# Kernel tuning notes

Hardware: AMD Instinct MI355X
Metric: run time of the kernel (lower is better)

The kernel has to match this reference:

```python
import jax, jax.numpy as jnp
import numpy as np

N = 100000      # nodes
E = 800000      # edges (nnz of sparse adj)
D_IN = 128      # input feature dim
H = 64          # hidden_units
EMB = 32        # embsize
N_IDX = 50000   # gathered output rows
EPS = 1e-05     # BatchNormalization epsilon


def spmm(rows, cols, vals, x):
    # out[i] = sum_{e: rows[e]==i} vals[e] * x[cols[e]]  == sparse A @ x
    return jax.ops.segment_sum(vals[:, None] * x[cols], rows, num_segments=N)


def batchnorm(x, gamma, beta):
    # training-mode BN over node (batch) axis, matching Keras BatchNormalization
    m = jnp.mean(x, axis=0)
    v = jnp.var(x, axis=0)
    return (x - m) * jax.lax.rsqrt(v + EPS) * gamma + beta


def setup_inputs() -> dict:
    key = jax.random.key(0)
    ks = jax.random.split(key, 16)
    def w(k, fan_in, shape):
        return jax.random.normal(k, shape, dtype=jnp.float32) / np.sqrt(fan_in)
    inp = {
        "features": jax.random.normal(ks[0], (N, D_IN), dtype=jnp.float32),
        "rows": jax.random.randint(ks[1], (E,), 0, N),
        "cols": jax.random.randint(ks[2], (E,), 0, N),
        "vals": jax.random.uniform(ks[3], (E,), dtype=jnp.float32),
        "idx": jax.random.randint(ks[4], (N_IDX,), 0, N),
        # layer 0 (Dense with bias since l==0)
        "Wn0": w(ks[5], D_IN, (D_IN, H)), "bn0": jnp.zeros((H,), jnp.float32),
        "Wg0": w(ks[6], D_IN, (D_IN, H)), "bg0": jnp.zeros((H,), jnp.float32),
        "ab0": jnp.zeros((H,), jnp.float32),  # BiasLayer after SpMM
        "g0": jnp.ones((H,), jnp.float32), "b0": jnp.zeros((H,), jnp.float32),
        # layer 1 (no Dense bias)
        "Wn1": w(ks[7], H, (H, H)),
        "Wg1": w(ks[8], H, (H, H)),
        "ab1": jnp.zeros((H,), jnp.float32),
        "g1": jnp.ones((H,), jnp.float32), "b1": jnp.zeros((H,), jnp.float32),
        # conv_last block (Dense use_bias=False)
        "WnL": w(ks[9], H, (H, EMB)),
        "WgL": w(ks[10], H, (H, EMB)),
        "abL": jnp.zeros((EMB,), jnp.float32),
    }
    return inp


def reference(features, rows, cols, vals, idx,
              Wn0, bn0, Wg0, bg0, ab0, g0, b0,
              Wn1, Wg1, ab1, g1, b1,
              WnL, WgL, abL):
    x = features
    # SAGE layer 0
    x_node = x @ Wn0 + bn0
    x_neigh = x @ Wg0 + bg0
    agg = spmm(rows, cols, vals, x_neigh) + ab0
    x = jax.nn.relu(batchnorm(x_node + agg, g0, b0))
    # SAGE layer 1
    x_node = x @ Wn1
    x_neigh = x @ Wg1
    agg = spmm(rows, cols, vals, x_neigh) + ab1
    x = jax.nn.relu(batchnorm(x_node + agg, g1, b1))
    # conv_last projection to embsize
    x_node = x @ WnL
    x_neigh = x @ WgL
    agg = spmm(rows, cols, vals, x_neigh) + abL
    x = x_node + agg
    return x[idx]
```

## Files before the change

### kernel.cpp

```cpp
#include <hip/hip_runtime.h>

#define NNODES 100000
#define NEDGES 800000
#define DIN    128
#define HID    64
#define EMB    32
#define NIDX   50000
#define BN_EPS 1e-5f

#define NCHK 64
#define EC   (NEDGES / NCHK)
#define SUBC 256
#define ECS  (NEDGES / SUBC)
#define SPC  (SUBC / NCHK)
#define NB   ((NNODES + 63) / 64)
#define PF   16
#define NBF  ((NB + PF - 1) / PF)

typedef __attribute__((ext_vector_type(8))) short short8;
typedef __attribute__((ext_vector_type(4))) float f32x4;

__device__ inline unsigned short f2bf(float f) {
    unsigned u = __float_as_uint(f);
    unsigned r = u + 0x7FFFu + ((u >> 16) & 1u);
    return (unsigned short)(r >> 16);
}
__device__ inline float bf2f_lo(unsigned u) { return __uint_as_float(u << 16); }
__device__ inline float bf2f_hi(unsigned u) { return __uint_as_float(u & 0xffff0000u); }


__device__ inline void pack_seg(const float* __restrict__ Wn, const float* __restrict__ Wg,
                                unsigned short* __restrict__ Wp, int HOUT, int l2nt, int f) {
    int j = f & 7, lane = (f >> 3) & 63, g = f >> 9;
    int tt = g & ((1 << l2nt) - 1), kb = g >> l2nt;
    int k = kb * 32 + ((lane >> 4) * 8) + j;
    int nn = tt * 16 + (lane & 15);
    float v = (nn < HOUT) ? Wn[k * HOUT + nn] : Wg[k * HOUT + (nn - HOUT)];
    Wp[f] = f2bf(v);
}


__global__ __launch_bounds__(256) void histpack_k(
    const int* __restrict__ rows, int* __restrict__ Bcnt4,
    const int* __restrict__ idx, int* __restrict__ mark,
    const float* Wn0, const float* Wg0, const float* Wn1,
    const float* Wg1, const float* WnL, const float* WgL,
    unsigned short* Wp0, unsigned short* Wp1, unsigned short* WpL, int MB)
{
    int blk = blockIdx.x;
    if (blk >= SUBC + MB) {
        int f = (blk - SUBC - MB) * 256 + threadIdx.x;
        if (f < 16384)      pack_seg(Wn0, Wg0, Wp0, 64, 3, f);
        else if (f < 24576) pack_seg(Wn1, Wg1, Wp1, 64, 3, f - 16384);
        else if (f < 28672) pack_seg(WnL, WgL, WpL, 32, 2, f - 24576);
        return;
    }
    if (blk >= SUBC) {
        int j = (blk - SUBC) * 256 + threadIdx.x;
        if (j < NIDX) mark[idx[j]] = 1;
        return;
    }
    __shared__ int hist[NB];
    int t = threadIdx.x;
    for (int b = t; b < NB; b += 256) hist[b] = 0;
    __syncthreads();
    for (int i = t; i < ECS; i += 256)
        atomicAdd(&hist[rows[blk * ECS + i] >> 6], 1);
    __syncthreads();
    for (int b = t; b < NB; b += 256) Bcnt4[blk * NB + b] = hist[b];
}

__global__ void bprefix_k(const int* __restrict__ Bcnt4, int* __restrict__ BcntT,
                          int* __restrict__ bTot) {
    int b = blockIdx.x * 256 + threadIdx.x;
    if (b >= NB) return;
    int run = 0;
    for (int sub = 0; sub < SUBC; sub++) {
        if ((sub & (SPC - 1)) == 0)
            BcntT[(sub / SPC) * NB + b] = run;
        run += Bcnt4[sub * NB + b];
    }
    bTot[b] = run;
}

__global__ void bscan_k(const int* __restrict__ bTot, int* __restrict__ bBase) {
    __shared__ int s[256];
    int t = threadIdx.x;
    int v[7], loc = 0;
#pragma unroll
    for (int i = 0; i < 7; i++) {
        int ix = t * 7 + i;
        v[i] = loc;
        loc += (ix < NB) ? bTot[ix] : 0;
    }
    s[t] = loc;
    __syncthreads();
    for (int off = 1; off < 256; off <<= 1) {
        int a = (t >= off) ? s[t - off] : 0;
        __syncthreads();
        s[t] += a;
        __syncthreads();
    }
    int base = s[t] - loc;
#pragma unroll
    for (int i = 0; i < 7; i++) {
        int ix = t * 7 + i;
        if (ix < NB) bBase[ix] = base + v[i];
    }
    if (t == 255) bBase[NB] = NEDGES;
}

__global__ __launch_bounds__(256) void bfinal_k(const uint2* __restrict__ ebuf,
                                                const int* __restrict__ bBase,
                                                int* __restrict__ rowptr,
                                                int2* __restrict__ cs) {
    __shared__ int hist[64], sc[64], cur[64];
    int b = blockIdx.x, t = threadIdx.x;
    int e0 = bBase[b], e1 = bBase[b + 1];
    int r0 = b << 6;
    if (t < 64) hist[t] = 0;
    __syncthreads();
    for (int i = e0 + t; i < e1; i += 256)
        atomicAdd(&hist[(ebuf[i].x >> 20) & 63], 1);
    __syncthreads();
    if (t == 0) {
        int run = e0;
        for (int j = 0; j < 64; j++) { sc[j] = run; run += hist[j]; }
    }
    __syncthreads();
    if (t < 64) {
        cur[t] = sc[t];
        int r = r0 + t;
        if (r < NNODES) rowptr[r] = sc[t];
    }
    if (b == NB - 1 && t == 0) rowptr[NNODES] = NEDGES;
    __syncthreads();
    for (int i = e0 + t; i < e1; i += 256) {
        uint2 v = ebuf[i];
        int p = atomicAdd(&cur[(v.x >> 20) & 63], 1);
        cs[p] = make_int2((int)(v.x & 0xFFFFF), (int)v.y);
    }
}


template <int K, int HOUT, bool AFF, bool XBF, bool HNBF>
__device__ void gemm_body(const void* __restrict__ Xv, const unsigned short* __restrict__ Wp,
                          const float* __restrict__ bnA, const float* __restrict__ bnB,
                          const float* __restrict__ bgA,
                          const float* __restrict__ sums, const float* __restrict__ gamma,
                          const float* __restrict__ beta,
                          float* __restrict__ Hnf, unsigned short* __restrict__ Hnb,
                          unsigned short* __restrict__ Hgb, int n, int blk)
{
    constexpr int NT = 2 * HOUT / 16, NKB = K / 32;
    constexpr int RS = K + 8;
    constexpr int OC = HNBF ? 2 * HOUT : HOUT;
    constexpr int RSE = OC + 8;
    constexpr int XSZ = (RS > RSE) ? RS : RSE;
    __shared__ unsigned short Xs[64 * XSZ];
    __shared__ float sSc[64], sSh[64];

    const int row0 = blk * 64;
    const int t = threadIdx.x;

    if (AFF) {
        if (t < 64) {
            float sum = 0.f, sq = 0.f;
#pragma unroll
            for (int s = 0; s < 8; s++) { sum += sums[s * 128 + t]; sq += sums[s * 128 + 64 + t]; }
            float m = sum / (float)NNODES;
            float var = sq / (float)NNODES - m * m;
            float sc = gamma[t] * rsqrtf(var + BN_EPS);
            sSc[t] = sc; sSh[t] = beta[t] - m * sc;
        }
        __syncthreads();
    }

    constexpr int SIT = K / 32;
    if constexpr (XBF) {
        uint4 u[SIT];
#pragma unroll
        for (int it = 0; it < SIT; it++) {
            int li = it * 256 + t;
            int rr = row0 + li / (K / 8);
            int k8 = (li % (K / 8)) * 8;
            int rc = rr < n ? rr : n - 1;
            u[it] = *(const uint4*)((const unsigned short*)Xv + (size_t)rc * K + k8);
        }
#pragma unroll
        for (int it = 0; it < SIT; it++) {
            int li = it * 256 + t;
            int r  = li / (K / 8);
            int k8 = (li % (K / 8)) * 8;
            float v[8];
            v[0] = bf2f_lo(u[it].x); v[1] = bf2f_hi(u[it].x);
            v[2] = bf2f_lo(u[it].y); v[3] = bf2f_hi(u[it].y);
            v[4] = bf2f_lo(u[it].z); v[5] = bf2f_hi(u[it].z);
            v[6] = bf2f_lo(u[it].w); v[7] = bf2f_hi(u[it].w);
            if (AFF) {
#pragma unroll
                for (int i = 0; i < 8; i++) v[i] = fmaxf(v[i] * sSc[k8 + i] + sSh[k8 + i], 0.f);
            }
            uint4 o;
            o.x = (unsigned)f2bf(v[0]) | ((unsigned)f2bf(v[1]) << 16);
            o.y = (unsigned)f2bf(v[2]) | ((unsigned)f2bf(v[3]) << 16);
            o.z = (unsigned)f2bf(v[4]) | ((unsigned)f2bf(v[5]) << 16);
            o.w = (unsigned)f2bf(v[6]) | ((unsigned)f2bf(v[7]) << 16);
            *(uint4*)&Xs[r * RS + k8] = o;
        }
    } else {
        const float* Xf = (const float*)Xv;
        float4 a[SIT], b[SIT];
#pragma unroll
        for (int it = 0; it < SIT; it++) {
            int li = it * 256 + t;
            int rr = row0 + li / (K / 8);
            int k8 = (li % (K / 8)) * 8;
            int rc = rr < n ? rr : n - 1;
            a[it] = *(const float4*)&Xf[(size_t)rc * K + k8];
            b[it] = *(const float4*)&Xf[(size_t)rc * K + k8 + 4];
        }
#pragma unroll
        for (int it = 0; it < SIT; it++) {
            int li = it * 256 + t;
            int r  = li / (K / 8);
            int k8 = (li % (K / 8)) * 8;
            float v[8] = { a[it].x, a[it].y, a[it].z, a[it].w,
                           b[it].x, b[it].y, b[it].z, b[it].w };
            if (AFF) {
#pragma unroll
                for (int i = 0; i < 8; i++) v[i] = fmaxf(v[i] * sSc[k8 + i] + sSh[k8 + i], 0.f);
            }
            uint4 o;
            o.x = (unsigned)f2bf(v[0]) | ((unsigned)f2bf(v[1]) << 16);
            o.y = (unsigned)f2bf(v[2]) | ((unsigned)f2bf(v[3]) << 16);
            o.z = (unsigned)f2bf(v[4]) | ((unsigned)f2bf(v[5]) << 16);
            o.w = (unsigned)f2bf(v[6]) | ((unsigned)f2bf(v[7]) << 16);
            *(uint4*)&Xs[r * RS + k8] = o;
        }
    }
    __syncthreads();

    const int wave = t >> 6, lane = t & 63;
    const int q = lane >> 4, mrow = lane & 15;

    f32x4 acc[NT];
#pragma unroll
    for (int i = 0; i < NT; i++) acc[i] = (f32x4){0.f, 0.f, 0.f, 0.f};

    const short8* wp8 = (const short8*)Wp;
#pragma unroll
    for (int kb = 0; kb < NKB; kb++) {
        short8 va = *(const short8*)&Xs[(wave * 16 + mrow) * RS + kb * 32 + q * 8];
#pragma unroll
        for (int tt = 0; tt < NT; tt++) {
            short8 vb = wp8[(kb * NT + tt) * 64 + lane];
            acc[tt] = __builtin_amdgcn_mfma_f32_16x16x32_bf16(va, vb, acc[tt], 0, 0, 0);
        }
    }

    __syncthreads();
#pragma unroll
    for (int tt = 0; tt < NT; tt++) {
        int nglob = tt * 16 + mrow;
        bool nside = (nglob < HOUT);
        int c = nside ? nglob : (nglob - HOUT);
        float bias = 0.f;
        if (nside) {
            if (bnA) bias += bnA[c];
            if (bnB) bias += bnB[c];
        } else if (bgA) {
            bias += bgA[c];
        }
        if (HNBF || !nside) {
            int cc = HNBF ? nglob : c;
#pragma unroll
            for (int r = 0; r < 4; r++)
                Xs[(wave * 16 + q * 4 + r) * RSE + cc] = f2bf(acc[tt][r] + bias);
        } else {
#pragma unroll
            for (int r = 0; r < 4; r++) {
                int rr = row0 + wave * 16 + q * 4 + r;
                if (rr < n) Hnf[(size_t)rr * HOUT + c] = acc[tt][r] + bias;
            }
        }
    }
    __syncthreads();
    constexpr int J = OC / 8;
#pragma unroll
    for (int u2 = 0; u2 < (64 * J) / 256; u2++) {
        int li = u2 * 256 + t;
        int r = li / J, j = li % J;
        int rr = row0 + r;
        if (rr < n) {
            uint4 v = *(const uint4*)&Xs[r * RSE + j * 8];
            int c8 = j * 8;
            if (HNBF && c8 < HOUT)
                *(uint4*)&Hnb[(size_t)rr * HOUT + c8] = v;
            else
                *(uint4*)&Hgb[(size_t)rr * HOUT + (HNBF ? c8 - HOUT : c8)] = v;
        }
    }
}

__global__ __launch_bounds__(256) void part_gemm0_k(
    const int* __restrict__ rows, const int* __restrict__ cols,
    const float* __restrict__ vals, const int* __restrict__ BcntT,
    const int* __restrict__ bBase, uint2* __restrict__ ebuf,
    const float* __restrict__ X, const unsigned short* __restrict__ Wp0,
    const float* __restrict__ bn0, const float* __restrict__ ab0, const float* __restrict__ bg0,
    unsigned short* __restrict__ Hn0b, unsigned short* __restrict__ Hgb, int n)
{
    if ((int)blockIdx.x < NCHK * PF) {
        __shared__ int cur[NBF];
        int t = threadIdx.x;
        int blk = blockIdx.x % NCHK;
        int pf  = blockIdx.x / NCHK;
        int b0 = pf * NBF, b1 = (pf == PF - 1) ? NB : (b0 + NBF);
        for (int b = b0 + t; b < b1; b += 256)
            cur[b - b0] = bBase[b] + BcntT[blk * NB + b];
        __syncthreads();
        constexpr int EC4 = EC / 4;
        const int* rbase = rows + blk * EC;
        for (int i4 = t; i4 < EC4; i4 += 256) {
            int4 r4 = *(const int4*)&rbase[i4 * 4];
            int e = blk * EC + i4 * 4;
#pragma unroll
            for (int j = 0; j < 4; j++) {
                int r = (&r4.x)[j];
                int b = r >> 6;
                if (b >= b0 && b < b1) {
                    int p = atomicAdd(&cur[b - b0], 1);
                    ebuf[p] = make_uint2(((unsigned)(r & 63) << 20) | (unsigned)cols[e + j],
                                         (unsigned)__float_as_int(vals[e + j]));
                }
            }
        }
    } else {
        gemm_body<DIN, HID, false, false, true>(X, Wp0, bn0, ab0, bg0,
            nullptr, nullptr, nullptr, nullptr, Hn0b, Hgb, n, blockIdx.x - NCHK * PF);
    }
}

template <int K, int HOUT, bool AFF, bool XBF, bool HNBF>
__global__ __launch_bounds__(256) void gemm_k(
    const void* __restrict__ X, const unsigned short* __restrict__ Wp,
    const float* __restrict__ bnA, const float* __restrict__ bnB, const float* __restrict__ bgA,
    const float* __restrict__ sums, const float* __restrict__ gamma, const float* __restrict__ beta,
    float* __restrict__ Hnf, unsigned short* __restrict__ Hnb, unsigned short* __restrict__ Hgb, int n)
{
    gemm_body<K, HOUT, AFF, XBF, HNBF>(X, Wp, bnA, bnB, bgA, sums, gamma, beta,
                                       Hnf, Hnb, Hgb, n, blockIdx.x);
}


template <int HH, bool STATS, bool SBF, bool MARKED>
__global__ __launch_bounds__(256) void spmm_k(
    const int* __restrict__ rowptr, const int2* __restrict__ cs,
    const unsigned short* __restrict__ Hgb, void* __restrict__ Sv,
    float* __restrict__ stats, const int* __restrict__ mark, int n)
{
    constexpr int L  = HH / 4;
    constexpr int GP = 256 / L;
    const int lane = threadIdx.x % L;
    const int g = threadIdx.x / L;
    const int gid = blockIdx.x * GP + g;
    const int ngroups = gridDim.x * GP;
    const int c0 = lane * 4;

    float4 sum = make_float4(0.f, 0.f, 0.f, 0.f);
    float4 sq  = make_float4(0.f, 0.f, 0.f, 0.f);
    for (int row = gid; row < n; row += ngroups) {
        if (MARKED && !mark[row]) continue;
        int e0 = rowptr[row], e1 = rowptr[row + 1];
        float4 a0, a1, a2, a3;
        if (SBF) {
            uint2 h = *(const uint2*)((const unsigned short*)Sv + (size_t)row * HH + c0);
            a0 = make_float4(bf2f_lo(h.x), bf2f_hi(h.x), bf2f_lo(h.y), bf2f_hi(h.y));
        } else {
            a0 = *(const float4*)((const float*)Sv + (size_t)row * HH + c0);
        }
        a1 = a2 = a3 = make_float4(0.f, 0.f, 0.f, 0.f);
        int e = e0;
        for (; e + 3 < e1; e += 4) {
            int2 p0 = cs[e], p1 = cs[e + 1], p2 = cs[e + 2], p3 = cs[e + 3];
            float v0 = __int_as_float(p0.y), v1 = __int_as_float(p1.y);
            float v2 = __int_as_float(p2.y), v3 = __int_as_float(p3.y);
            uint2 h0 = *(const uint2*)&Hgb[(size_t)p0.x * HH + c0];
            uint2 h1 = *(const uint2*)&Hgb[(size_t)p1.x * HH + c0];
            uint2 h2 = *(const uint2*)&Hgb[(size_t)p2.x * HH + c0];
            uint2 h3 = *(const uint2*)&Hgb[(size_t)p3.x * HH + c0];
            a0.x += v0 * bf2f_lo(h0.x); a0.y += v0 * bf2f_hi(h0.x);
            a0.z += v0 * bf2f_lo(h0.y); a0.w += v0 * bf2f_hi(h0.y);
            a1.x += v1 * bf2f_lo(h1.x); a1.y += v1 * bf2f_hi(h1.x);
            a1.z += v1 * bf2f_lo(h1.y); a1.w += v1 * bf2f_hi(h1.y);
            a2.x += v2 * bf2f_lo(h2.x); a2.y += v2 * bf2f_hi(h2.x);
            a2.z += v2 * bf2f_lo(h2.y); a2.w += v2 * bf2f_hi(h2.y);
            a3.x += v3 * bf2f_lo(h3.x); a3.y += v3 * bf2f_hi(h3.x);
            a3.z += v3 * bf2f_lo(h3.y); a3.w += v3 * bf2f_hi(h3.y);
        }
        for (; e < e1; e++) {
            int2 p = cs[e];
            float v = __int_as_float(p.y);
            uint2 h = *(const uint2*)&Hgb[(size_t)p.x * HH + c0];
            a0.x += v * bf2f_lo(h.x); a0.y += v * bf2f_hi(h.x);
            a0.z += v * bf2f_lo(h.y); a0.w += v * bf2f_hi(h.y);
        }
        float4 acc = make_float4(a0.x + a1.x + a2.x + a3.x, a0.y + a1.y + a2.y + a3.y,
                                 a0.z + a1.z + a2.z + a3.z, a0.w + a1.w + a2.w + a3.w);
        if (SBF) {
            uint2 o;
            o.x = (unsigned)f2bf(acc.x) | ((unsigned)f2bf(acc.y) << 16);
            o.y = (unsigned)f2bf(acc.z) | ((unsigned)f2bf(acc.w) << 16);
            *(uint2*)((unsigned short*)Sv + (size_t)row * HH + c0) = o;
        } else {
            *(float4*)((float*)Sv + (size_t)row * HH + c0) = acc;
        }
        if (STATS) {
            sum.x += acc.x; sum.y += acc.y; sum.z += acc.z; sum.w += acc.w;
            sq.x += acc.x * acc.x; sq.y += acc.y * acc.y;
            sq.z += acc.z * acc.z; sq.w += acc.w * acc.w;
        }
    }

    if constexpr (STATS) {
        __shared__ float rs[GP][HH];
        __shared__ float rq[GP][HH];
        *(float4*)&rs[g][c0] = sum;
        *(float4*)&rq[g][c0] = sq;
        __syncthreads();
        if (threadIdx.x < HH) {
            float a = 0.f, b = 0.f;
            for (int w = 0; w < GP; w++) { a += rs[w][threadIdx.x]; b += rq[w][threadIdx.x]; }
            int stripe = blockIdx.x & 7;
            atomicAdd(&stats[stripe * 128 + threadIdx.x], a);
            atomicAdd(&stats[stripe * 128 + HH + threadIdx.x], b);
        }
    }
}

__global__ void gather_k(const float* __restrict__ S, const int* __restrict__ idx,
                         float* __restrict__ out, int total4) {
    int j = blockIdx.x * 256 + threadIdx.x;
    if (j < total4) {
        int r = j / (EMB / 4), c4 = (j % (EMB / 4)) * 4;
        *(float4*)&out[(size_t)j * 4] = *(const float4*)&S[(size_t)idx[r] * EMB + c4];
    }
}


extern "C" void kernel_launch(void* const* d_in, const int* in_sizes, int n_in,
                              void* d_out, int out_size, void* d_ws, size_t ws_size,
                              hipStream_t stream) {
    const float* features = (const float*)d_in[0];
    const int*   rows     = (const int*)d_in[1];
    const int*   cols     = (const int*)d_in[2];
    const float* vals     = (const float*)d_in[3];
    const int*   idx      = (const int*)d_in[4];
    const float* Wn0 = (const float*)d_in[5];
    const float* bn0 = (const float*)d_in[6];
    const float* Wg0 = (const float*)d_in[7];
    const float* bg0 = (const float*)d_in[8];
    const float* ab0 = (const float*)d_in[9];
    const float* g0  = (const float*)d_in[10];
    const float* b0  = (const float*)d_in[11];
    const float* Wn1 = (const float*)d_in[12];
    const float* Wg1 = (const float*)d_in[13];
    const float* ab1 = (const float*)d_in[14];
    const float* g1  = (const float*)d_in[15];
    const float* b1  = (const float*)d_in[16];
    const float* WnL = (const float*)d_in[17];
    const float* WgL = (const float*)d_in[18];
    const float* abL = (const float*)d_in[19];
    float* out = (float*)d_out;

    float*          HnLf = (float*)d_ws;
    unsigned short* nA   = (unsigned short*)(HnLf + (size_t)NNODES * EMB);
    unsigned short* nB   = nA + (size_t)NNODES * HID;
    unsigned short* Hgb  = nB + (size_t)NNODES * HID;
    uint2* ebuf  = (uint2*)(Hgb + (size_t)NNODES * HID);
    int2*  cs    = (int2*)(ebuf + NEDGES);
    int*   rowptr = (int*)(cs + NEDGES);
    int*   Bcnt4 = rowptr + (NNODES + 4);
    int*   BcntT = Bcnt4 + SUBC * NB;
    int*   bTot  = BcntT + NCHK * NB;
    int*   bBase = bTot + 1568;
    unsigned short* Wp0 = (unsigned short*)(bBase + 1568);
    unsigned short* Wp1 = Wp0 + 16384;
    unsigned short* WpL = Wp1 + 8192;
    float* stats = (float*)(WpL + 4096);
    int*   mark  = (int*)(stats + 2304);
    float* sums0 = stats;
    float* sums1 = stats + 1024;
    size_t zbytes = 2304 * 4 + (size_t)NNODES * 4;

    hipMemsetAsync(stats, 0, zbytes, stream);

    const int GBm = (NNODES + 63) / 64;
    const int MB  = (NIDX + 255) / 256;

    histpack_k<<<SUBC + MB + 112, 256, 0, stream>>>(
        rows, Bcnt4, idx, mark, Wn0, Wg0, Wn1, Wg1, WnL, WgL, Wp0, Wp1, WpL, MB);
    bprefix_k<<<7, 256, 0, stream>>>(Bcnt4, BcntT, bTot);
    bscan_k<<<1, 256, 0, stream>>>(bTot, bBase);
    part_gemm0_k<<<NCHK * PF + GBm, 256, 0, stream>>>(rows, cols, vals, BcntT, bBase, ebuf,
                                                      features, Wp0, bn0, ab0, bg0,
                                                      nA, Hgb, NNODES);
    bfinal_k<<<NB, 256, 0, stream>>>(ebuf, bBase, rowptr, cs);

    spmm_k<HID, true, true, false><<<1600, 256, 0, stream>>>(rowptr, cs, Hgb, nA, sums0, nullptr, NNODES);

    gemm_k<HID, HID, true, true, true><<<GBm, 256, 0, stream>>>(
        nA, Wp1, ab1, nullptr, nullptr, sums0, g0, b0, nullptr, nB, Hgb, NNODES);
    spmm_k<HID, true, true, false><<<1600, 256, 0, stream>>>(rowptr, cs, Hgb, nB, sums1, nullptr, NNODES);

    gemm_k<HID, EMB, true, true, false><<<GBm, 256, 0, stream>>>(
        nB, WpL, abL, nullptr, nullptr, sums1, g1, b1, HnLf, nullptr, Hgb, NNODES);
    spmm_k<EMB, false, false, true><<<1600, 256, 0, stream>>>(rowptr, cs, Hgb, HnLf, nullptr, mark, NNODES);

    gather_k<<<(NIDX * EMB / 4 + 255) / 256, 256, 0, stream>>>(HnLf, idx, out, NIDX * EMB / 4);
}
```

Baseline: 290.1 us.

## Stage per-block edge lists in LDS for SpMM and vectorize partition loads

SpMM now gives each block a fixed contiguous range of 64 rows. The block stages that range's row pointers and up to 1024 CSR edges in shared memory with coalesced loads, and rows whose edges overflow fall back to global reads. The old grid-stride loop over a fixed 1600-block grid is replaced by one launch sized by node blocks. Separately, the partition kernel loads cols and vals as 4-wide vectors alongside rows instead of doing scalar loads per edge. The aim is to cut scattered, uncoalesced index loads, at the cost of extra barriers and LDS use per block.

```diff
diff --git a/kernel.cpp b/kernel.cpp
--- a/kernel.cpp
+++ b/kernel.cpp
@@ -321,18 +321,21 @@
             cur[b - b0] = bBase[b] + BcntT[blk * NB + b];
         __syncthreads();
         constexpr int EC4 = EC / 4;
-        const int* rbase = rows + blk * EC;
+        const int*   rbase = rows + blk * EC;
+        const int*   cbase = cols + blk * EC;
+        const float* vbase = vals + blk * EC;
         for (int i4 = t; i4 < EC4; i4 += 256) {
-            int4 r4 = *(const int4*)&rbase[i4 * 4];
-            int e = blk * EC + i4 * 4;
+            int4   r4 = *(const int4*)&rbase[i4 * 4];
+            int4   c4 = *(const int4*)&cbase[i4 * 4];
+            float4 v4 = *(const float4*)&vbase[i4 * 4];
 #pragma unroll
             for (int j = 0; j < 4; j++) {
                 int r = (&r4.x)[j];
                 int b = r >> 6;
                 if (b >= b0 && b < b1) {
                     int p = atomicAdd(&cur[b - b0], 1);
-                    ebuf[p] = make_uint2(((unsigned)(r & 63) << 20) | (unsigned)cols[e + j],
-                                         (unsigned)__float_as_int(vals[e + j]));
+                    ebuf[p] = make_uint2(((unsigned)(r & 63) << 20) | (unsigned)(&c4.x)[j],
+                                         (unsigned)__float_as_int((&v4.x)[j]));
                 }
             }
         }
@@ -360,19 +363,68 @@
     const unsigned short* __restrict__ Hgb, void* __restrict__ Sv,
     float* __restrict__ stats, const int* __restrict__ mark, int n)
 {
-    constexpr int L  = HH / 4;
-    constexpr int GP = 256 / L;
-    const int lane = threadIdx.x % L;
-    const int g = threadIdx.x / L;
-    const int gid = blockIdx.x * GP + g;
-    const int ngroups = gridDim.x * GP;
-    const int c0 = lane * 4;
+    constexpr int L   = HH / 4;
+    constexpr int GP  = 256 / L;
+    constexpr int RPB = 64;
+    constexpr int RPG = RPB / GP;
+    constexpr int ECAP = 1024;
+    __shared__ int2 es[ECAP];
+    __shared__ int  rp[RPB + 1];
+
+    const int t = threadIdx.x;
+    const int R0 = blockIdx.x * RPB;
+    if (t <= RPB) rp[t] = rowptr[min(R0 + t, n)];
+    __syncthreads();
+    const int e0b  = rp[0];
+    const int scnt = min(rp[RPB] - e0b, ECAP);
+    for (int i = t; i < scnt; i += 256) es[i] = cs[e0b + i];
+    __syncthreads();
+
+    const int lane = t % L;
+    const int g    = t / L;
+    const int c0   = lane * 4;
 
     float4 sum = make_float4(0.f, 0.f, 0.f, 0.f);
     float4 sq  = make_float4(0.f, 0.f, 0.f, 0.f);
-    for (int row = gid; row < n; row += ngroups) {
+
+#define SPMM_ROW(FETCH)                                                            \
+    {                                                                              \
+        int e = le0;                                                               \
+        for (; e + 3 < le1; e += 4) {                                              \
+            int2 p0 = FETCH(e), p1 = FETCH(e + 1), p2 = FETCH(e + 2), p3 = FETCH(e + 3); \
+            float v0 = __int_as_float(p0.y), v1 = __int_as_float(p1.y);            \
+            float v2 = __int_as_float(p2.y), v3 = __int_as_float(p3.y);            \
+            uint2 h0 = *(const uint2*)&Hgb[(size_t)p0.x * HH + c0];                \
+            uint2 h1 = *(const uint2*)&Hgb[(size_t)p1.x * HH + c0];                \
+            uint2 h2 = *(const uint2*)&Hgb[(size_t)p2.x * HH + c0];                \
+            uint2 h3 = *(const uint2*)&Hgb[(size_t)p3.x * HH + c0];                \
+            a0.x += v0 * bf2f_lo(h0.x); a0.y += v0 * bf2f_hi(h0.x);                \
+            a0.z += v0 * bf2f_lo(h0.y); a0.w += v0 * bf2f_hi(h0.y);                \
+            a1.x += v1 * bf2f_lo(h1.x); a1.y += v1 * bf2f_hi(h1.x);                \
+            a1.z += v1 * bf2f_lo(h1.y); a1.w += v1 * bf2f_hi(h1.y);                \
+            a2.x += v2 * bf2f_lo(h2.x); a2.y += v2 * bf2f_hi(h2.x);                \
+            a2.z += v2 * bf2f_lo(h2.y); a2.w += v2 * bf2f_hi(h2.y);                \
+            a3.x += v3 * bf2f_lo(h3.x); a3.y += v3 * bf2f_hi(h3.x);                \
+            a3.z += v3 * bf2f_lo(h3.y); a3.w += v3 * bf2f_hi(h3.y);                \
+        }                                                                          \
+        for (; e < le1; e++) {                                                     \
+            int2 p = FETCH(e);                                                     \
+            float v = __int_as_float(p.y);                                         \
+            uint2 h = *(const uint2*)&Hgb[(size_t)p.x * HH + c0];                  \
+            a0.x += v * bf2f_lo(h.x); a0.y += v * bf2f_hi(h.x);                    \
+            a0.z += v * bf2f_lo(h.y); a0.w += v * bf2f_hi(h.y);                    \
+        }                                                                          \
+    }
+#define F_LDS(i) es[(i)]
+#define F_GLB(i) cs[e0b + (i)]
+
+#pragma unroll
+    for (int rr = 0; rr < RPG; rr++) {
+        int row = R0 + g * RPG + rr;
+        if (row >= n) break;
         if (MARKED && !mark[row]) continue;
-        int e0 = rowptr[row], e1 = rowptr[row + 1];
+        int le0 = rp[g * RPG + rr] - e0b;
+        int le1 = rp[g * RPG + rr + 1] - e0b;
         float4 a0, a1, a2, a3;
         if (SBF) {
             uint2 h = *(const uint2*)((const unsigned short*)Sv + (size_t)row * HH + c0);
@@ -381,31 +433,7 @@
             a0 = *(const float4*)((const float*)Sv + (size_t)row * HH + c0);
         }
         a1 = a2 = a3 = make_float4(0.f, 0.f, 0.f, 0.f);
-        int e = e0;
-        for (; e + 3 < e1; e += 4) {
-            int2 p0 = cs[e], p1 = cs[e + 1], p2 = cs[e + 2], p3 = cs[e + 3];
-            float v0 = __int_as_float(p0.y), v1 = __int_as_float(p1.y);
-            float v2 = __int_as_float(p2.y), v3 = __int_as_float(p3.y);
-            uint2 h0 = *(const uint2*)&Hgb[(size_t)p0.x * HH + c0];
-            uint2 h1 = *(const uint2*)&Hgb[(size_t)p1.x * HH + c0];
-            uint2 h2 = *(const uint2*)&Hgb[(size_t)p2.x * HH + c0];
-            uint2 h3 = *(const uint2*)&Hgb[(size_t)p3.x * HH + c0];
-            a0.x += v0 * bf2f_lo(h0.x); a0.y += v0 * bf2f_hi(h0.x);
-            a0.z += v0 * bf2f_lo(h0.y); a0.w += v0 * bf2f_hi(h0.y);
-            a1.x += v1 * bf2f_lo(h1.x); a1.y += v1 * bf2f_hi(h1.x);
-            a1.z += v1 * bf2f_lo(h1.y); a1.w += v1 * bf2f_hi(h1.y);
-            a2.x += v2 * bf2f_lo(h2.x); a2.y += v2 * bf2f_hi(h2.x);
-            a2.z += v2 * bf2f_lo(h2.y); a2.w += v2 * bf2f_hi(h2.y);
-            a3.x += v3 * bf2f_lo(h3.x); a3.y += v3 * bf2f_hi(h3.x);
-            a3.z += v3 * bf2f_lo(h3.y); a3.w += v3 * bf2f_hi(h3.y);
-        }
-        for (; e < e1; e++) {
-            int2 p = cs[e];
-            float v = __int_as_float(p.y);
-            uint2 h = *(const uint2*)&Hgb[(size_t)p.x * HH + c0];
-            a0.x += v * bf2f_lo(h.x); a0.y += v * bf2f_hi(h.x);
-            a0.z += v * bf2f_lo(h.y); a0.w += v * bf2f_hi(h.y);
-        }
+        if (le1 <= scnt) SPMM_ROW(F_LDS) else SPMM_ROW(F_GLB);
         float4 acc = make_float4(a0.x + a1.x + a2.x + a3.x, a0.y + a1.y + a2.y + a3.y,
                                  a0.z + a1.z + a2.z + a3.z, a0.w + a1.w + a2.w + a3.w);
         if (SBF) {
@@ -422,6 +450,9 @@
             sq.z += acc.z * acc.z; sq.w += acc.w * acc.w;
         }
     }
+#undef SPMM_ROW
+#undef F_LDS
+#undef F_GLB
 
     if constexpr (STATS) {
         __shared__ float rs[GP][HH];
@@ -508,15 +539,15 @@
                                                       nA, Hgb, NNODES);
     bfinal_k<<<NB, 256, 0, stream>>>(ebuf, bBase, rowptr, cs);
 
-    spmm_k<HID, true, true, false><<<1600, 256, 0, stream>>>(rowptr, cs, Hgb, nA, sums0, nullptr, NNODES);
+    spmm_k<HID, true, true, false><<<GBm, 256, 0, stream>>>(rowptr, cs, Hgb, nA, sums0, nullptr, NNODES);
 
     gemm_k<HID, HID, true, true, true><<<GBm, 256, 0, stream>>>(
         nA, Wp1, ab1, nullptr, nullptr, sums0, g0, b0, nullptr, nB, Hgb, NNODES);
-    spmm_k<HID, true, true, false><<<1600, 256, 0, stream>>>(rowptr, cs, Hgb, nB, sums1, nullptr, NNODES);
+    spmm_k<HID, true, true, false><<<GBm, 256, 0, stream>>>(rowptr, cs, Hgb, nB, sums1, nullptr, NNODES);
 
     gemm_k<HID, EMB, true, true, false><<<GBm, 256, 0, stream>>>(
         nB, WpL, abL, nullptr, nullptr, sums1, g1, b1, HnLf, nullptr, Hgb, NNODES);
-    spmm_k<EMB, false, false, true><<<1600, 256, 0, stream>>>(rowptr, cs, Hgb, HnLf, nullptr, mark, NNODES);
+    spmm_k<EMB, false, false, true><<<GBm, 256, 0, stream>>>(rowptr, cs, Hgb, HnLf, nullptr, mark, NNODES);
 
     gather_k<<<(NIDX * EMB / 4 + 255) / 256, 256, 0, stream>>>(HnLf, idx, out, NIDX * EMB / 4);
 }
```

Result: faster. 278.0 us (-4.2%).
